# Kernel tuning notes

Hardware: AMD Instinct MI355X
Metric: run time of the kernel (lower is better)

The kernel has to match this reference:

```python
import jax, jax.numpy as jnp
import numpy as np

N_NODES = 100000
N_EDGES = 1000000
IN_CH = 64
OUT_CH = 16


def setup_inputs() -> dict:
    key = jax.random.key(0)
    ks = jax.random.split(key, 6)
    x = jax.random.normal(ks[0], (N_NODES, IN_CH), dtype=jnp.float32)
    W1 = jax.random.normal(ks[1], (IN_CH, IN_CH), dtype=jnp.float32) / np.sqrt(IN_CH)
    b1 = jax.random.normal(ks[2], (IN_CH,), dtype=jnp.float32) * 0.01
    W2 = jax.random.normal(ks[3], (IN_CH, OUT_CH), dtype=jnp.float32) / np.sqrt(IN_CH)
    b2 = jax.random.normal(ks[4], (OUT_CH,), dtype=jnp.float32) * 0.01
    edge_index = jax.random.randint(ks[5], (2, N_EDGES), 0, N_NODES, dtype=jnp.int64)
    return {"x": x, "W1": W1, "b1": b1, "W2": W2, "b2": b2,
            "edge_index": edge_index, "K": 3}


def _gcn_conv(x, W, b, src, dst, norm, n_nodes):
    # GCNConv: out = scatter_add(norm * (x @ W)[src], dst) + b
    h = x @ W                                   # [N, d_out]
    msg = h[src] * norm[:, None]                # [E+N, d_out] edge-wise gather
    agg = jax.ops.segment_sum(msg, dst, num_segments=n_nodes)
    return agg + b


def reference(x, W1, b1, W2, b2, edge_index, K):
    n = x.shape[0]
    loops = jnp.arange(n, dtype=edge_index.dtype)
    src = jnp.concatenate([edge_index[0], loops])  # A_hat = A + I
    dst = jnp.concatenate([edge_index[1], loops])
    # symmetric normalization deg^{-1/2} A_hat deg^{-1/2}
    deg = jnp.zeros((n,), dtype=x.dtype).at[dst].add(1.0)
    dinv = jax.lax.rsqrt(deg)  # deg >= 1 thanks to self-loops
    norm = dinv[src] * dinv[dst]
    for _ in range(K):
        x = _gcn_conv(x, W1, b1, src, dst, norm, n)
    return _gcn_conv(x, W2, b2, src, dst, norm, n)
```

## Files before the change

### kernel.cpp

```cpp
#include <hip/hip_runtime.h>
#include <hip/hip_bf16.h>
#include <stdint.h>

__device__ __forceinline__ float bf2f(unsigned short u) {
    unsigned int x = ((unsigned int)u) << 16;
    return __uint_as_float(x);
}
__device__ __forceinline__ unsigned short f2bf(float f) {
    unsigned int x = __float_as_uint(f);
    unsigned int lsb = (x >> 16) & 1u;
    x += 0x7fffu + lsb;
    return (unsigned short)(x >> 16);
}
__device__ __forceinline__ unsigned int pack2bf(float lo, float hi) {
    return (unsigned int)f2bf(lo) | ((unsigned int)f2bf(hi) << 16);
}
__device__ __forceinline__ float bflo(unsigned int u) { return __uint_as_float(u << 16); }
__device__ __forceinline__ float bfhi(unsigned int u) { return __uint_as_float(u & 0xffff0000u); }
__device__ __forceinline__ float loadF(const void* p, int i, int isbf) {
    return isbf ? bf2f(((const unsigned short*)p)[i]) : ((const float*)p)[i];
}

__global__ void k_init(const void* x, const void* eidx, int* flags, int* bcnt, int B,
                       unsigned int* z0s, unsigned int* z1s) {
    int t = threadIdx.x;
    for (int b = t; b < B; b += blockDim.x) bcnt[b] = 0;
    if (t < 8) z0s[t] = 0;
    else if (t < 16) z1s[t - 8] = 0;
    if (t < 64) {
        const unsigned short* u = (const unsigned short*)x;
        float a = fabsf(bf2f(u[2 * t]));
        bool ok = (a == 0.0f) || (a > 1e-30f && a < 1e4f);
        unsigned long long mbf = __ballot(ok);
        if (t == 0) flags[0] = (mbf == ~0ULL) ? 1 : 0;
    } else if (t < 128) {
        int l = t - 64;
        const int* ip = (const int*)eidx;
        unsigned long long mi64 = __ballot(ip[2 * l + 1] == 0);
        if (l == 0) flags[1] = (mi64 == ~0ULL) ? 1 : 0;
    }
}

#define TS 68
__global__ void k_bin(const void* eidx, int E, int rsh, int B, int cap,
                      unsigned int* bins, int* bcnt, const int* flags,
                      const void* W1, const void* b1, const void* W2, const void* b2,
                      float* M, float* cvecs, int nbin) {
    if ((int)blockIdx.x == nbin) {
        __shared__ float A[64 * 64];
        __shared__ float T1[64 * TS];
        __shared__ float T2[64 * TS];
        __shared__ float B2s[64 * 16];
        __shared__ float bv[64], bw1[64], bw2[64];
        int bf = flags[0];
        int t = threadIdx.x;
        if (t < 256) {
            for (int i = t; i < 4096; i += 256) A[i] = loadF(W1, i, bf);
            for (int i = t; i < 1024; i += 256) B2s[i] = loadF(W2, i, bf);
            if (t < 64) bv[t] = loadF(b1, t, bf);
        }
        __syncthreads();
        if (t < 256) {
            const int i0 = (t >> 4) * 4;
            const int j0 = (t & 15) * 4;
            {
                float acc[4][4] = {};
#pragma unroll 8
                for (int k = 0; k < 64; ++k) {
                    float a0 = A[(i0 + 0) * 64 + k];
                    float a1 = A[(i0 + 1) * 64 + k];
                    float a2 = A[(i0 + 2) * 64 + k];
                    float a3 = A[(i0 + 3) * 64 + k];
                    float4 bq = *(const float4*)&A[k * 64 + j0];
                    acc[0][0] += a0 * bq.x; acc[0][1] += a0 * bq.y; acc[0][2] += a0 * bq.z; acc[0][3] += a0 * bq.w;
                    acc[1][0] += a1 * bq.x; acc[1][1] += a1 * bq.y; acc[1][2] += a1 * bq.z; acc[1][3] += a1 * bq.w;
                    acc[2][0] += a2 * bq.x; acc[2][1] += a2 * bq.y; acc[2][2] += a2 * bq.z; acc[2][3] += a2 * bq.w;
                    acc[3][0] += a3 * bq.x; acc[3][1] += a3 * bq.y; acc[3][2] += a3 * bq.z; acc[3][3] += a3 * bq.w;
                }
#pragma unroll
                for (int ii = 0; ii < 4; ++ii)
                    *(float4*)&T1[(i0 + ii) * TS + j0] = make_float4(acc[ii][0], acc[ii][1], acc[ii][2], acc[ii][3]);
            }
            if (t < 64) {
                float acc = 0.f;
#pragma unroll 8
                for (int i = 0; i < 64; ++i) acc += bv[i] * A[i * 64 + t];
                bw1[t] = acc;
            }
        }
        __syncthreads();
        if (t < 256) {
            const int i0 = (t >> 4) * 4;
            const int j0 = (t & 15) * 4;
            {
                float acc[4][4] = {};
#pragma unroll 8
                for (int k = 0; k < 64; ++k) {
                    float a0 = T1[(i0 + 0) * TS + k];
                    float a1 = T1[(i0 + 1) * TS + k];
                    float a2 = T1[(i0 + 2) * TS + k];
                    float a3 = T1[(i0 + 3) * TS + k];
                    float4 bq = *(const float4*)&A[k * 64 + j0];
                    acc[0][0] += a0 * bq.x; acc[0][1] += a0 * bq.y; acc[0][2] += a0 * bq.z; acc[0][3] += a0 * bq.w;
                    acc[1][0] += a1 * bq.x; acc[1][1] += a1 * bq.y; acc[1][2] += a1 * bq.z; acc[1][3] += a1 * bq.w;
                    acc[2][0] += a2 * bq.x; acc[2][1] += a2 * bq.y; acc[2][2] += a2 * bq.z; acc[2][3] += a2 * bq.w;
                    acc[3][0] += a3 * bq.x; acc[3][1] += a3 * bq.y; acc[3][2] += a3 * bq.z; acc[3][3] += a3 * bq.w;
                }
#pragma unroll
                for (int ii = 0; ii < 4; ++ii)
                    *(float4*)&T2[(i0 + ii) * TS + j0] = make_float4(acc[ii][0], acc[ii][1], acc[ii][2], acc[ii][3]);
            }
            if (t < 64) {
                float acc = 0.f;
#pragma unroll 8
                for (int i = 0; i < 64; ++i) acc += bw1[i] * A[i * 64 + t];
                bw2[t] = acc;
            }
        }
        __syncthreads();
        if (t < 256) {
            {
                int i = t >> 2, j0m = (t & 3) * 4;
                float4 acc = {0.f, 0.f, 0.f, 0.f};
#pragma unroll 8
                for (int k = 0; k < 64; ++k) {
                    float a = T2[i * TS + k];
                    float4 bq = *(const float4*)&B2s[k * 16 + j0m];
                    acc.x += a * bq.x; acc.y += a * bq.y; acc.z += a * bq.z; acc.w += a * bq.w;
                }
                *(float4*)&M[i * 16 + j0m] = acc;
            }
            if (t < 16) {
                float a3 = 0.f, a2 = 0.f, a1 = 0.f;
#pragma unroll 8
                for (int i = 0; i < 64; ++i) {
                    float w = B2s[i * 16 + t];
                    a3 += bw2[i] * w;
                    a2 += bw1[i] * w;
                    a1 += bv[i] * w;
                }
                cvecs[t] = a3;
                cvecs[16 + t] = a2;
                cvecs[32 + t] = a1;
                cvecs[48 + t] = loadF(b2, t, flags[0]);
            }
        }
        return;
    }
    extern __shared__ int sh[];
    int* hist   = sh;
    int* base_s = sh + B;
    const int i64 = flags[1];
    const int t = threadIdx.x, nt = blockDim.x;
    const long long i0 = (long long)blockIdx.x * E / nbin;
    const long long i1 = (long long)(blockIdx.x + 1) * E / nbin;
    const long long* e64 = (const long long*)eidx;
    const int* e32 = (const int*)eidx;
    const int mask = (1 << rsh) - 1;

    for (int b = t; b < B; b += nt) hist[b] = 0;
    __syncthreads();
    for (long long i = i0 + t; i < i1; i += nt) {
        int d = i64 ? (int)e64[E + i] : e32[E + i];
        atomicAdd(&hist[d >> rsh], 1);
    }
    __syncthreads();
    for (int b = t; b < B; b += nt) {
        int c = hist[b];
        base_s[b] = c ? atomicAdd(&bcnt[b], c) : 0;
        hist[b] = 0;
    }
    __syncthreads();
    for (long long i = i0 + t; i < i1; i += nt) {
        int d, s;
        if (i64) { d = (int)e64[E + i]; s = (int)e64[i]; }
        else     { d = e32[E + i];     s = e32[i]; }
        int b = d >> rsh;
        int pos = base_s[b] + atomicAdd(&hist[b], 1);
        if (pos >= cap) pos = cap - 1;
        bins[(size_t)b * cap + pos] = ((unsigned int)s << rsh) | (unsigned int)(d & mask);
    }
}

__global__ void k_csr(const unsigned int* bins, const int* bcnt, int cap, int capP,
                      int rsh, int n, int* colb, int4* meta) {
    __shared__ int dh[128], db[128], pl[128], ch[128];
    const int R = 1 << rsh;
    const int b = blockIdx.x, t = threadIdx.x, nt = blockDim.x;
    const int mask = R - 1;
    for (int r = t; r < R; r += nt) { dh[r] = 0; ch[r] = 0; }
    __syncthreads();
    int cnt = bcnt[b]; if (cnt > cap) cnt = cap;
    const unsigned int* eb = bins + (size_t)b * cap;
    for (int e = t; e < cnt; e += nt)
        atomicAdd(&dh[eb[e] & mask], 1);
    __syncthreads();
    if (t < R) { pl[t] = (dh[t] + 3) & ~3; db[t] = pl[t]; }
    __syncthreads();
    for (int off = 1; off < R; off <<= 1) {
        int add = 0;
        if (t < R && t >= off) add = db[t - off];
        __syncthreads();
        if (t < R) db[t] += add;
        __syncthreads();
    }
    const int v0 = b << rsh;
    const int gbase = b * capP;
    if (t < R) {
        int v = v0 + t;
        if (v < n) {
            int len = dh[t];
            float dv = rsqrtf((float)(len + 1));
            int rs = gbase + db[t] - pl[t];
            meta[v] = make_int4(rs, len, __float_as_int(dv), 0);
            for (int p = len; p < pl[t]; ++p) colb[rs + p] = n;
        }
    }
    __syncthreads();
    for (int e = t; e < cnt; e += nt) {
        unsigned int w = eb[e];
        int r = w & mask;
        int pos = (db[r] - pl[r]) + atomicAdd(&ch[r], 1);
        colb[gbase + pos] = (int)(w >> rsh);
    }
}

__global__ void k_xm(const void* x, const float* M, const int4* meta,
                     unsigned short* z0, int n, const int* flags) {
    __shared__ float Ms[64 * 16];
    __shared__ float xs[16 * 64];
    int bf = flags[0];
    int t = threadIdx.x;
    ((float4*)Ms)[t] = ((const float4*)M)[t];
    int base = blockIdx.x * 16;
    if (!bf) {
        int row = base + (t >> 4);
        float4 v = make_float4(0.f, 0.f, 0.f, 0.f);
        if (row < n) v = ((const float4*)x)[base * 16 + t];
        ((float4*)xs)[t] = v;
    } else {
        for (int k = t; k < 1024; k += 256) {
            int r = k >> 6, cc = k & 63;
            int row = base + r;
            xs[k] = (row < n) ? bf2f(((const unsigned short*)x)[row * 64 + cc]) : 0.f;
        }
    }
    __syncthreads();
    int r = t >> 4, c = t & 15;
    int row = base + r;
    if (row < n) {
        float acc = 0.f;
#pragma unroll
        for (int k = 0; k < 64; ++k) acc += xs[r * 64 + k] * Ms[k * 16 + c];
        float dv = __int_as_float(meta[row].z);
        z0[row * 16 + c] = f2bf(dv * acc);
    }
}

__global__ void k_prop(const unsigned short* zin, void* yout, const int4* meta,
                       const int* colb, const float* cvec,
                       int n, int is_final, const int* flags) {
    int tid = blockIdx.x * blockDim.x + threadIdx.x;
    int v = tid >> 1, h = tid & 1;
    if (v >= n) return;
    int4 m = meta[v];
    int beg = m.x, len = m.y;
    int padlen = (len + 3) & ~3;
    int4 sw = *(const int4*)&zin[(size_t)v * 16 + h * 8];
    float a0 = bflo((unsigned)sw.x), a1 = bfhi((unsigned)sw.x);
    float a2 = bflo((unsigned)sw.y), a3 = bfhi((unsigned)sw.y);
    float a4 = bflo((unsigned)sw.z), a5 = bfhi((unsigned)sw.z);
    float a6 = bflo((unsigned)sw.w), a7 = bfhi((unsigned)sw.w);
    for (int j = beg; j < beg + padlen; j += 4) {
        int4 cc = *(const int4*)&colb[j];
        int4 za = *(const int4*)&zin[(size_t)cc.x * 16 + h * 8];
        int4 zb = *(const int4*)&zin[(size_t)cc.y * 16 + h * 8];
        int4 zc = *(const int4*)&zin[(size_t)cc.z * 16 + h * 8];
        int4 zd = *(const int4*)&zin[(size_t)cc.w * 16 + h * 8];
        a0 += (bflo((unsigned)za.x) + bflo((unsigned)zb.x)) + (bflo((unsigned)zc.x) + bflo((unsigned)zd.x));
        a1 += (bfhi((unsigned)za.x) + bfhi((unsigned)zb.x)) + (bfhi((unsigned)zc.x) + bfhi((unsigned)zd.x));
        a2 += (bflo((unsigned)za.y) + bflo((unsigned)zb.y)) + (bflo((unsigned)zc.y) + bflo((unsigned)zd.y));
        a3 += (bfhi((unsigned)za.y) + bfhi((unsigned)zb.y)) + (bfhi((unsigned)zc.y) + bfhi((unsigned)zd.y));
        a4 += (bflo((unsigned)za.z) + bflo((unsigned)zb.z)) + (bflo((unsigned)zc.z) + bflo((unsigned)zd.z));
        a5 += (bfhi((unsigned)za.z) + bfhi((unsigned)zb.z)) + (bfhi((unsigned)zc.z) + bfhi((unsigned)zd.z));
        a6 += (bflo((unsigned)za.w) + bflo((unsigned)zb.w)) + (bflo((unsigned)zc.w) + bflo((unsigned)zd.w));
        a7 += (bfhi((unsigned)za.w) + bfhi((unsigned)zb.w)) + (bfhi((unsigned)zc.w) + bfhi((unsigned)zd.w));
    }
    float dv = __int_as_float(m.z);
    float sa = is_final ? dv : dv * dv;
    float sb = is_final ? 1.0f : dv;
    float4 cv0 = *(const float4*)&cvec[h * 8];
    float4 cv1 = *(const float4*)&cvec[h * 8 + 4];
    float r0 = sa * a0 + sb * cv0.x;
    float r1 = sa * a1 + sb * cv0.y;
    float r2 = sa * a2 + sb * cv0.z;
    float r3 = sa * a3 + sb * cv0.w;
    float r4 = sa * a4 + sb * cv1.x;
    float r5 = sa * a5 + sb * cv1.y;
    float r6 = sa * a6 + sb * cv1.z;
    float r7 = sa * a7 + sb * cv1.w;
    if (is_final) {
        if (flags[0]) {
            int4 ov;
            ov.x = (int)pack2bf(r0, r1);
            ov.y = (int)pack2bf(r2, r3);
            ov.z = (int)pack2bf(r4, r5);
            ov.w = (int)pack2bf(r6, r7);
            *(int4*)&((unsigned short*)yout)[(size_t)v * 16 + h * 8] = ov;
        } else {
            float* o = &((float*)yout)[(size_t)v * 16 + h * 8];
            *(float4*)o = make_float4(r0, r1, r2, r3);
            *(float4*)(o + 4) = make_float4(r4, r5, r6, r7);
        }
    } else {
        int4 ov;
        ov.x = (int)pack2bf(r0, r1);
        ov.y = (int)pack2bf(r2, r3);
        ov.z = (int)pack2bf(r4, r5);
        ov.w = (int)pack2bf(r6, r7);
        *(int4*)&((unsigned short*)yout)[(size_t)v * 16 + h * 8] = ov;
    }
}

extern "C" void kernel_launch(void* const* d_in, const int* in_sizes, int n_in,
                              void* d_out, int out_size, void* d_ws, size_t ws_size,
                              hipStream_t stream) {
    const void* x  = d_in[0];
    const void* W1 = d_in[1];
    const void* b1 = d_in[2];
    const void* W2 = d_in[3];
    const void* b2 = d_in[4];
    const void* ei = d_in[5];

    const int n = in_sizes[0] / 64;
    const int E = in_sizes[5] / 2;

    const int rsh = 7;
    const int B = (n + (1 << rsh) - 1) >> rsh;
    const int avg = E / B;
    int cap = avg + avg / 4 + 128;
    cap = (cap + 31) & ~31;
    const int capP = cap + 512;

    char* base = (char*)d_ws;
    size_t off = 0;
    auto carve = [&](size_t bytes) -> void* {
        void* r = base + off;
        off = (off + bytes + 255) & ~(size_t)255;
        return r;
    };
    int*            flags  = (int*)carve(8);
    int*            bcnt   = (int*)carve((size_t)B * 4);
    unsigned int*   bins   = (unsigned int*)carve((size_t)B * cap * 4);
    int*            colb   = (int*)carve((size_t)B * capP * 4);
    int4*           meta   = (int4*)carve((size_t)n * 16);
    float*          Mm     = (float*)carve(1024 * 4);
    float*          cvecs  = (float*)carve(64 * 4);
    unsigned short* z0     = (unsigned short*)carve(((size_t)n + 1) * 16 * 2);
    unsigned short* z1     = (unsigned short*)carve(((size_t)n + 1) * 16 * 2);
    (void)ws_size; (void)n_in; (void)out_size;

    const int nbin = 240;
    k_init<<<1, 1024, 0, stream>>>(x, ei, flags, bcnt, B,
                                   (unsigned int*)&z0[(size_t)n * 16],
                                   (unsigned int*)&z1[(size_t)n * 16]);
    k_bin<<<nbin + 1, 512, (size_t)2 * B * 4, stream>>>(ei, E, rsh, B, cap, bins, bcnt,
                                                        flags, W1, b1, W2, b2, Mm, cvecs, nbin);
    k_csr<<<B, 256, 0, stream>>>(bins, bcnt, cap, capP, rsh, n, colb, meta);
    k_xm<<<(n + 15) / 16, 256, 0, stream>>>(x, Mm, meta, z0, n, flags);

    const int pgrid = (n * 2 + 255) / 256;
    k_prop<<<pgrid, 256, 0, stream>>>(z0, z1, meta, colb, cvecs + 0,  n, 0, flags);
    k_prop<<<pgrid, 256, 0, stream>>>(z1, z0, meta, colb, cvecs + 16, n, 0, flags);
    k_prop<<<pgrid, 256, 0, stream>>>(z0, z1, meta, colb, cvecs + 32, n, 0, flags);
    k_prop<<<pgrid, 256, 0, stream>>>(z1, d_out, meta, colb, cvecs + 48, n, 1, flags);
}
```

Before: 102.1 us.

## Bin edges into per-block private buckets and fuse feature transform into CSR build

The binning pass drops its separate histogram/global-atomic reservation phase. Each block now writes edges straight into a private fixed-capacity segment per (bucket, block), and overflow goes to a global spill list. The CSR kernel gathers and compacts these segments in shared memory, scans them, builds rows, and also performs the x@M projection for its 128 nodes, which removes the separate k_xm launch. The aim is to cut one pass over edge_index, the global atomics and one kernel launch. In exchange it adds a serial per-thread segment copy, a scan of the spill list in every block, and hard caps (2048 edges per bucket, fixed capP) that could truncate on skewed graphs.

```diff
diff --git a/kernel.cpp b/kernel.cpp
--- a/kernel.cpp
+++ b/kernel.cpp
@@ -1,6 +1,12 @@
 #include <hip/hip_runtime.h>
 #include <hip/hip_bf16.h>
 #include <stdint.h>
+
+#define NBIN 240
+#define RSH 7
+#define RNODES 128
+#define SPILLCAP 16384
+#define TS 68
 
 __device__ __forceinline__ float bf2f(unsigned short u) {
     unsigned int x = ((unsigned int)u) << 16;
@@ -21,12 +27,12 @@
     return isbf ? bf2f(((const unsigned short*)p)[i]) : ((const float*)p)[i];
 }
 
-__global__ void k_init(const void* x, const void* eidx, int* flags, int* bcnt, int B,
+__global__ void k_init(const void* x, const void* eidx, int* flags,
                        unsigned int* z0s, unsigned int* z1s) {
     int t = threadIdx.x;
-    for (int b = t; b < B; b += blockDim.x) bcnt[b] = 0;
     if (t < 8) z0s[t] = 0;
     else if (t < 16) z1s[t - 8] = 0;
+    if (t == 16) flags[2] = 0;
     if (t < 64) {
         const unsigned short* u = (const unsigned short*)x;
         float a = fabsf(bf2f(u[2 * t]));
@@ -41,12 +47,11 @@
     }
 }
 
-#define TS 68
-__global__ void k_bin(const void* eidx, int E, int rsh, int B, int cap,
-                      unsigned int* bins, int* bcnt, const int* flags,
+__global__ void k_bin(const void* eidx, int E, int B, int capBB,
+                      unsigned int* bins, int* cnts, int* flags, int2* spill,
                       const void* W1, const void* b1, const void* W2, const void* b2,
-                      float* M, float* cvecs, int nbin) {
-    if ((int)blockIdx.x == nbin) {
+                      float* M, float* cvecs) {
+    if ((int)blockIdx.x == NBIN) {
         __shared__ float A[64 * 64];
         __shared__ float T1[64 * TS];
         __shared__ float T2[64 * TS];
@@ -147,66 +152,102 @@
         }
         return;
     }
-    extern __shared__ int sh[];
-    int* hist   = sh;
-    int* base_s = sh + B;
+    extern __shared__ int hist[];
     const int i64 = flags[1];
     const int t = threadIdx.x, nt = blockDim.x;
-    const long long i0 = (long long)blockIdx.x * E / nbin;
-    const long long i1 = (long long)(blockIdx.x + 1) * E / nbin;
+    const int blk = blockIdx.x;
+    const long long i0 = (long long)blk * E / NBIN;
+    const long long i1 = (long long)(blk + 1) * E / NBIN;
     const long long* e64 = (const long long*)eidx;
     const int* e32 = (const int*)eidx;
-    const int mask = (1 << rsh) - 1;
+    const int mask = RNODES - 1;
 
     for (int b = t; b < B; b += nt) hist[b] = 0;
-    __syncthreads();
-    for (long long i = i0 + t; i < i1; i += nt) {
-        int d = i64 ? (int)e64[E + i] : e32[E + i];
-        atomicAdd(&hist[d >> rsh], 1);
-    }
-    __syncthreads();
-    for (int b = t; b < B; b += nt) {
-        int c = hist[b];
-        base_s[b] = c ? atomicAdd(&bcnt[b], c) : 0;
-        hist[b] = 0;
-    }
     __syncthreads();
     for (long long i = i0 + t; i < i1; i += nt) {
         int d, s;
         if (i64) { d = (int)e64[E + i]; s = (int)e64[i]; }
         else     { d = e32[E + i];     s = e32[i]; }
-        int b = d >> rsh;
-        int pos = base_s[b] + atomicAdd(&hist[b], 1);
-        if (pos >= cap) pos = cap - 1;
-        bins[(size_t)b * cap + pos] = ((unsigned int)s << rsh) | (unsigned int)(d & mask);
-    }
-}
-
-__global__ void k_csr(const unsigned int* bins, const int* bcnt, int cap, int capP,
-                      int rsh, int n, int* colb, int4* meta) {
-    __shared__ int dh[128], db[128], pl[128], ch[128];
-    const int R = 1 << rsh;
+        int b = d >> RSH;
+        unsigned int pk = ((unsigned int)s << RSH) | (unsigned int)(d & mask);
+        int pos = atomicAdd(&hist[b], 1);
+        if (pos < capBB) {
+            bins[(size_t)(b * NBIN + blk) * capBB + pos] = pk;
+        } else {
+            int sp = atomicAdd(&flags[2], 1);
+            if (sp < SPILLCAP) spill[sp] = make_int2(b, (int)pk);
+        }
+    }
+    __syncthreads();
+    for (int b = t; b < B; b += nt) {
+        int c = hist[b];
+        cnts[b * NBIN + blk] = c > capBB ? capBB : c;
+    }
+}
+
+__global__ void k_csr(const unsigned int* bins, const int* cnts, int capBB,
+                      const int* flags, const int2* spill,
+                      int n, int* colb, int capP, int4* meta,
+                      const void* x, const float* M, unsigned short* z0) {
+    __shared__ int compact[2048];
+    __shared__ int scnt[NBIN], sof[NBIN];
+    __shared__ int dh[RNODES], db[RNODES], pl[RNODES], ch[RNODES];
+    __shared__ float Ms[1024];
+    __shared__ float xs[RNODES * 65];
+    __shared__ int sextra;
     const int b = blockIdx.x, t = threadIdx.x, nt = blockDim.x;
-    const int mask = R - 1;
-    for (int r = t; r < R; r += nt) { dh[r] = 0; ch[r] = 0; }
-    __syncthreads();
-    int cnt = bcnt[b]; if (cnt > cap) cnt = cap;
-    const unsigned int* eb = bins + (size_t)b * cap;
-    for (int e = t; e < cnt; e += nt)
-        atomicAdd(&dh[eb[e] & mask], 1);
-    __syncthreads();
-    if (t < R) { pl[t] = (dh[t] + 3) & ~3; db[t] = pl[t]; }
-    __syncthreads();
-    for (int off = 1; off < R; off <<= 1) {
+    const int mask = RNODES - 1;
+    if (t < NBIN) { int c = cnts[b * NBIN + t]; scnt[t] = c > capBB ? capBB : c; }
+    if (t < RNODES) { dh[t] = 0; ch[t] = 0; }
+    if (t == 0) sextra = 0;
+    __syncthreads();
+    if (t < NBIN) sof[t] = scnt[t];
+    __syncthreads();
+    for (int off = 1; off < NBIN; off <<= 1) {
         int add = 0;
-        if (t < R && t >= off) add = db[t - off];
-        __syncthreads();
-        if (t < R) db[t] += add;
-        __syncthreads();
-    }
-    const int v0 = b << rsh;
+        if (t < NBIN && t >= off) add = sof[t - off];
+        __syncthreads();
+        if (t < NBIN) sof[t] += add;
+        __syncthreads();
+    }
+    int total = sof[NBIN - 1];
+    if (t < NBIN) {
+        const unsigned int* seg = bins + (size_t)(b * NBIN + t) * capBB;
+        int dst = sof[t] - scnt[t];
+        for (int i = 0; i < scnt[t]; ++i) compact[dst + i] = (int)seg[i];
+    }
+    {
+        int scount = flags[2];
+        if (scount > SPILLCAP) scount = SPILLCAP;
+        for (int i = t; i < scount; i += nt) {
+            int2 sp = spill[i];
+            if (sp.x == b) {
+                int p = atomicAdd(&sextra, 1);
+                if (total + p < 2048) compact[total + p] = sp.y;
+            }
+        }
+    }
+    __syncthreads();
+    {
+        int ex = sextra;
+        if (total + ex > 2048) ex = 2048 - total;
+        total += ex;
+    }
+    for (int e = t; e < total; e += nt)
+        atomicAdd(&dh[compact[e] & mask], 1);
+    __syncthreads();
+    if (t < RNODES) { pl[t] = (dh[t] + 3) & ~3; db[t] = pl[t]; }
+    __syncthreads();
+    for (int off = 1; off < RNODES; off <<= 1) {
+        int add = 0;
+        if (t < RNODES && t >= off) add = db[t - off];
+        __syncthreads();
+        if (t < RNODES) db[t] += add;
+        __syncthreads();
+    }
+    const int v0 = b << RSH;
     const int gbase = b * capP;
-    if (t < R) {
+    if (t < RNODES) {
         int v = v0 + t;
         if (v < n) {
             int len = dh[t];
@@ -217,43 +258,57 @@
         }
     }
     __syncthreads();
-    for (int e = t; e < cnt; e += nt) {
-        unsigned int w = eb[e];
+    for (int e = t; e < total; e += nt) {
+        int w = compact[e];
         int r = w & mask;
         int pos = (db[r] - pl[r]) + atomicAdd(&ch[r], 1);
-        colb[gbase + pos] = (int)(w >> rsh);
-    }
-}
-
-__global__ void k_xm(const void* x, const float* M, const int4* meta,
-                     unsigned short* z0, int n, const int* flags) {
-    __shared__ float Ms[64 * 16];
-    __shared__ float xs[16 * 64];
-    int bf = flags[0];
-    int t = threadIdx.x;
+        colb[gbase + pos] = w >> RSH;
+    }
+    const int bf = flags[0];
     ((float4*)Ms)[t] = ((const float4*)M)[t];
-    int base = blockIdx.x * 16;
-    if (!bf) {
-        int row = base + (t >> 4);
-        float4 v = make_float4(0.f, 0.f, 0.f, 0.f);
-        if (row < n) v = ((const float4*)x)[base * 16 + t];
-        ((float4*)xs)[t] = v;
-    } else {
-        for (int k = t; k < 1024; k += 256) {
-            int r = k >> 6, cc = k & 63;
-            int row = base + r;
-            xs[k] = (row < n) ? bf2f(((const unsigned short*)x)[row * 64 + cc]) : 0.f;
-        }
-    }
-    __syncthreads();
-    int r = t >> 4, c = t & 15;
-    int row = base + r;
-    if (row < n) {
-        float acc = 0.f;
-#pragma unroll
-        for (int k = 0; k < 64; ++k) acc += xs[r * 64 + k] * Ms[k * 16 + c];
-        float dv = __int_as_float(meta[row].z);
-        z0[row * 16 + c] = f2bf(dv * acc);
+    int nvalid = n - v0;
+    if (nvalid > RNODES) nvalid = RNODES;
+    if (nvalid > 0) {
+        if (!bf) {
+            const float* xf = (const float*)x + (size_t)v0 * 64;
+            for (int i = t; i < nvalid * 16; i += nt) {
+                int r = i >> 4, c4 = (i & 15) * 4;
+                float4 v = *(const float4*)&xf[r * 64 + c4];
+                float* xp = &xs[r * 65 + c4];
+                xp[0] = v.x; xp[1] = v.y; xp[2] = v.z; xp[3] = v.w;
+            }
+        } else {
+            const unsigned short* xu = (const unsigned short*)x + (size_t)v0 * 64;
+            for (int i = t; i < nvalid * 16; i += nt) {
+                int r = i >> 4, c4 = (i & 15) * 4;
+                ushort4 v = *(const ushort4*)&xu[r * 64 + c4];
+                float* xp = &xs[r * 65 + c4];
+                xp[0] = bf2f(v.x); xp[1] = bf2f(v.y); xp[2] = bf2f(v.z); xp[3] = bf2f(v.w);
+            }
+        }
+    }
+    __syncthreads();
+    {
+        int r = t >> 1, h = t & 1;
+        int v = v0 + r;
+        if (v < n) {
+            float a0 = 0.f, a1 = 0.f, a2 = 0.f, a3 = 0.f;
+            float a4 = 0.f, a5 = 0.f, a6 = 0.f, a7 = 0.f;
+#pragma unroll 8
+            for (int k = 0; k < 64; ++k) {
+                float xv = xs[r * 65 + k];
+                const float* mp = &Ms[k * 16 + h * 8];
+                a0 += xv * mp[0]; a1 += xv * mp[1]; a2 += xv * mp[2]; a3 += xv * mp[3];
+                a4 += xv * mp[4]; a5 += xv * mp[5]; a6 += xv * mp[6]; a7 += xv * mp[7];
+            }
+            float dv = rsqrtf((float)(dh[r] + 1));
+            int4 ov;
+            ov.x = (int)pack2bf(dv * a0, dv * a1);
+            ov.y = (int)pack2bf(dv * a2, dv * a3);
+            ov.z = (int)pack2bf(dv * a4, dv * a5);
+            ov.w = (int)pack2bf(dv * a6, dv * a7);
+            *(int4*)&z0[(size_t)v * 16 + h * 8] = ov;
+        }
     }
 }
 
@@ -299,19 +354,10 @@
     float r5 = sa * a5 + sb * cv1.y;
     float r6 = sa * a6 + sb * cv1.z;
     float r7 = sa * a7 + sb * cv1.w;
-    if (is_final) {
-        if (flags[0]) {
-            int4 ov;
-            ov.x = (int)pack2bf(r0, r1);
-            ov.y = (int)pack2bf(r2, r3);
-            ov.z = (int)pack2bf(r4, r5);
-            ov.w = (int)pack2bf(r6, r7);
-            *(int4*)&((unsigned short*)yout)[(size_t)v * 16 + h * 8] = ov;
-        } else {
-            float* o = &((float*)yout)[(size_t)v * 16 + h * 8];
-            *(float4*)o = make_float4(r0, r1, r2, r3);
-            *(float4*)(o + 4) = make_float4(r4, r5, r6, r7);
-        }
+    if (is_final && !flags[0]) {
+        float* o = &((float*)yout)[(size_t)v * 16 + h * 8];
+        *(float4*)o = make_float4(r0, r1, r2, r3);
+        *(float4*)(o + 4) = make_float4(r4, r5, r6, r7);
     } else {
         int4 ov;
         ov.x = (int)pack2bf(r0, r1);
@@ -334,13 +380,8 @@
 
     const int n = in_sizes[0] / 64;
     const int E = in_sizes[5] / 2;
-
-    const int rsh = 7;
-    const int B = (n + (1 << rsh) - 1) >> rsh;
-    const int avg = E / B;
-    int cap = avg + avg / 4 + 128;
-    cap = (cap + 31) & ~31;
-    const int capP = cap + 512;
+    const int B = (n + RNODES - 1) >> RSH;
+    const int capP = 2432;
 
     char* base = (char*)d_ws;
     size_t off = 0;
@@ -349,25 +390,30 @@
         off = (off + bytes + 255) & ~(size_t)255;
         return r;
     };
-    int*            flags  = (int*)carve(8);
-    int*            bcnt   = (int*)carve((size_t)B * 4);
-    unsigned int*   bins   = (unsigned int*)carve((size_t)B * cap * 4);
-    int*            colb   = (int*)carve((size_t)B * capP * 4);
-    int4*           meta   = (int4*)carve((size_t)n * 16);
-    float*          Mm     = (float*)carve(1024 * 4);
-    float*          cvecs  = (float*)carve(64 * 4);
-    unsigned short* z0     = (unsigned short*)carve(((size_t)n + 1) * 16 * 2);
-    unsigned short* z1     = (unsigned short*)carve(((size_t)n + 1) * 16 * 2);
-    (void)ws_size; (void)n_in; (void)out_size;
-
-    const int nbin = 240;
-    k_init<<<1, 1024, 0, stream>>>(x, ei, flags, bcnt, B,
-                                   (unsigned int*)&z0[(size_t)n * 16],
-                                   (unsigned int*)&z1[(size_t)n * 16]);
-    k_bin<<<nbin + 1, 512, (size_t)2 * B * 4, stream>>>(ei, E, rsh, B, cap, bins, bcnt,
-                                                        flags, W1, b1, W2, b2, Mm, cvecs, nbin);
-    k_csr<<<B, 256, 0, stream>>>(bins, bcnt, cap, capP, rsh, n, colb, meta);
-    k_xm<<<(n + 15) / 16, 256, 0, stream>>>(x, Mm, meta, z0, n, flags);
+    int*            flags = (int*)carve(16);
+    int*            cnts  = (int*)carve((size_t)NBIN * B * 4);
+    int2*           spill = (int2*)carve((size_t)SPILLCAP * 8);
+    int*            colb  = (int*)carve((size_t)B * capP * 4);
+    int4*           meta  = (int4*)carve((size_t)n * 16);
+    float*          Mm    = (float*)carve(1024 * 4);
+    float*          cvecs = (float*)carve(64 * 4);
+    unsigned short* z0    = (unsigned short*)carve(((size_t)n + 1) * 16 * 2);
+    unsigned short* z1    = (unsigned short*)carve(((size_t)n + 1) * 16 * 2);
+    size_t remain = (ws_size > off) ? (ws_size - off) : 0;
+    int capBB = (int)(remain / ((size_t)NBIN * B * 4));
+    if (capBB > 28) capBB = 28;
+    if (capBB < 12) capBB = 12;
+    unsigned int* bins = (unsigned int*)carve((size_t)NBIN * B * capBB * 4);
+    (void)n_in; (void)out_size;
+
+    k_init<<<1, 128, 0, stream>>>(x, ei, flags,
+                                  (unsigned int*)&z0[(size_t)n * 16],
+                                  (unsigned int*)&z1[(size_t)n * 16]);
+    k_bin<<<NBIN + 1, 512, (size_t)B * 4, stream>>>(ei, E, B, capBB, bins, cnts,
+                                                    flags, spill,
+                                                    W1, b1, W2, b2, Mm, cvecs);
+    k_csr<<<B, 256, 0, stream>>>(bins, cnts, capBB, flags, spill,
+                                 n, colb, capP, meta, x, Mm, z0);
 
     const int pgrid = (n * 2 + 255) / 256;
     k_prop<<<pgrid, 256, 0, stream>>>(z0, z1, meta, colb, cvecs + 0,  n, 0, flags);
```

Result: slower. 108.0 us (+5.8%).
